# Performance work log

Measured on AMD Instinct MI355X. Metric: run time of the kernel, lower is better.

## Reference

```python
import jax, jax.numpy as jnp
import numpy as np
from jax import lax

EPOCHS = 3
N_IN, N_OUT = 20, 18
BN_EPS = 1e-5
RECT_EPS = 1e-4
TRIU = np.triu_indices(N_OUT)  # SPDVectorize upper-triangular indices


def _orth(key, n, m):
    # Stiefel init: orthonormal columns, like nn.init.orthogonal_
    q, _ = jnp.linalg.qr(jax.random.normal(key, (n, m), dtype=jnp.float32))
    return q


def setup_inputs() -> dict:
    key = jax.random.key(0)
    ks = jax.random.split(key, 8)
    bs = 2048
    f32 = jnp.float32
    return dict(
        x=jax.random.normal(ks[0], (bs, 1, 22, 438), dtype=f32),
        W1=jax.random.normal(ks[1], (22, 1, 22, 1), dtype=f32) * 0.1,
        b1=jnp.zeros((22,), f32),
        g1=jnp.ones((22,), f32), be1=jnp.zeros((22,), f32),
        W2=jax.random.normal(ks[2], (20, 22, 1, 12), dtype=f32) * 0.05,
        b2=jnp.zeros((20,), f32),
        g2=jnp.ones((20,), f32), be2=jnp.zeros((20,), f32),
        Wq=_orth(ks[3], N_IN, N_OUT),
        Wk=_orth(ks[4], N_IN, N_OUT),
        Wv=_orth(ks[5], N_IN, N_OUT),
        Wl=jax.random.normal(ks[6], (N_OUT * (N_OUT + 1) // 2 * EPOCHS, 4), dtype=f32) * 0.02,
        bl=jnp.zeros((4,), f32),
    )


def _bn(x, g, b):
    # BatchNorm2d forward in training mode (batch statistics, biased var)
    mean = x.mean(axis=(0, 2, 3), keepdims=True)
    var = ((x - mean) ** 2).mean(axis=(0, 2, 3), keepdims=True)
    return (x - mean) * lax.rsqrt(var + BN_EPS) * g[None, :, None, None] + b[None, :, None, None]


def _conv(x, w, b, pad_w):
    y = lax.conv_general_dilated(x, w, (1, 1), [(0, 0), (pad_w, pad_w)],
                                 dimension_numbers=('NCHW', 'OIHW', 'NCHW'))
    return y + b[None, :, None, None]


def _signal2spd(x):
    # x: (bs, C, L) -> trace-normalized covariance + 1e-5 * I
    L = x.shape[-1]
    xc = x - x.mean(-1, keepdims=True)
    cov = jnp.einsum('bcl,bdl->bcd', xc, xc) / (L - 1)
    cov = cov / jnp.trace(cov, axis1=-2, axis2=-1)[:, None, None]
    return cov + 1e-5 * jnp.eye(cov.shape[-1], dtype=cov.dtype)


def _patch_lens(n, epochs):
    base = n // epochs
    lens = [base] * epochs
    for i in range(n - base * epochs):
        lens[i] += 1
    return lens


def _spd_fn(t, fn):
    # SPD functional calculus via eigh (== torch.svd on SPD input)
    s, u = jnp.linalg.eigh(t)
    return jnp.einsum('...ij,...j,...kj->...ik', u, fn(s), u)


def _forward(x, W1, b1, g1, be1, W2, b2, g2, be2, Wq, Wk, Wv, Wl, bl):
    bs = x.shape[0]
    h = _bn(_conv(x, W1, b1, 0), g1, be1)          # (bs,22,1,438)
    h = _bn(_conv(h, W2, b2, 6), g2, be2)          # (bs,20,1,439)
    sig = h[:, :, 0, :]                            # squeeze -> (bs,20,439)
    covs, off = [], 0
    for L in _patch_lens(sig.shape[-1], EPOCHS):   # E2R: [147,146,146]
        covs.append(_signal2spd(sig[:, :, off:off + L]))
        off += L
    X = jnp.stack(covs, axis=1)                    # (bs,m,20,20) SPD
    # SPDTransform: W^T X W with Stiefel W (20,18)
    Q = jnp.einsum('pi,bmpq,qj->bmij', Wq, X, Wq)
    K = jnp.einsum('pi,bmpq,qj->bmij', Wk, X, Wk)
    V = jnp.einsum('pi,bmpq,qj->bmij', Wv, X, Wv)
    logQ = _spd_fn(Q, jnp.log)
    logK = _spd_fn(K, jnp.log)
    logV = _spd_fn(V, jnp.log)
    # log-Euclidean distance^2: ||log Q_j - log K_i||_F^2  (== sum of svd singvals of D D^T)
    diff = logQ[:, :, None] - logK[:, None, :]     # (bs, mq, mk, n, n)
    energy = jnp.sum(diff * diff, axis=(-2, -1))   # (bs, mq, mk)
    scores = 1.0 / (1.0 + jnp.log1p(energy))
    # torch: softmax over dim=-2 then permute(0,2,1) == softmax over K index here
    P = jax.nn.softmax(scores, axis=-1)            # (bs, mq, mk)
    mixed = jnp.einsum('bji,bipq->bjpq', P, logV)  # weighted log-Euclidean mean
    out = _spd_fn(mixed, jnp.exp)
    out = _spd_fn(out, lambda s: jnp.maximum(s, RECT_EPS))  # SPDRectified
    logO = _spd_fn(out, jnp.log)                   # SPDTangentSpace log
    vec = logO[..., TRIU[0], TRIU[1]]              # (bs, m, 171)
    return vec.reshape(bs, -1) @ Wl + bl           # (bs, 4)


def reference(x, W1, b1, g1, be1, W2, b2, g2, be2, Wq, Wk, Wv, Wl, bl):
    return _forward(x, W1, b1, g1, be1, W2, b2, g2, be2, Wq, Wk, Wv, Wl, bl)
```

## Files before the change

### kernel.cpp

```cpp
#include <hip/hip_runtime.h>
#include <math.h>

#define OFF_Y2   0
#define OFF_QKV  17981440
#define OFF_ST   (17981440 + 5971968)
#define ST_SX   0
#define ST_SXX  22
#define ST_WF   506
#define ST_BF   990
#define ST_Y2S  1012
#define ST_Y2Q  1032
#define ST_TOT  1052

#define LOGEPS -9.210340371976182f
#define NSWEEP 5
#define SHIFT  12.0f

__global__ __launch_bounds__(256) void k0_zero(float* __restrict__ st){
  for (int i = threadIdx.x; i < ST_TOT; i += 256) st[i] = 0.f;
}

__global__ __launch_bounds__(256) void k1_xstats(const float* __restrict__ x, float* __restrict__ st){
  __shared__ __align__(16) float xs[22*444];
  const float* xb = x + (size_t)blockIdx.x * (22*438);
  for (int i = threadIdx.x; i < 22*444; i += 256){
    int h = i / 444, w = i - h*444;
    xs[i] = (w < 438) ? xb[h*438 + w] : 0.f;
  }
  __syncthreads();
  for (int t = threadIdx.x; t < 275; t += 256){
    if (t < 22){
      const float4* r = (const float4*)&xs[t*444];
      float4 acc = {0.f,0.f,0.f,0.f};
      for (int w = 0; w < 111; ++w){ float4 v = r[w]; acc.x+=v.x; acc.y+=v.y; acc.z+=v.z; acc.w+=v.w; }
      atomicAdd(&st[ST_SX + t], acc.x+acc.y+acc.z+acc.w);
    } else {
      int rem = t - 22, h = 0;
      while (rem >= 22 - h){ rem -= 22 - h; ++h; }
      int h2 = h + rem;
      const float4* ra = (const float4*)&xs[h*444];
      const float4* rb = (const float4*)&xs[h2*444];
      float4 acc = {0.f,0.f,0.f,0.f};
      for (int w = 0; w < 111; ++w){
        float4 a = ra[w], b = rb[w];
        acc.x = fmaf(a.x,b.x,acc.x); acc.y = fmaf(a.y,b.y,acc.y);
        acc.z = fmaf(a.z,b.z,acc.z); acc.w = fmaf(a.w,b.w,acc.w);
      }
      atomicAdd(&st[ST_SXX + h*22 + h2], acc.x+acc.y+acc.z+acc.w);
    }
  }
}

__global__ __launch_bounds__(64) void k1b_fold(const float* __restrict__ W1, const float* __restrict__ g1,
                                               const float* __restrict__ be1, float* __restrict__ st){
  int c = threadIdx.x;
  if (c >= 22) return;
  const float invN = 1.f / (2048.f*438.f);
  float mcol[22];
  float mu0 = 0.f;
  for (int h = 0; h < 22; ++h){ mcol[h] = W1[c*22 + h]; mu0 = fmaf(mcol[h], st[ST_SX + h], mu0); }
  mu0 *= invN;
  float qf = 0.f;
  for (int h = 0; h < 22; ++h)
    for (int h2 = h; h2 < 22; ++h2){
      float w = mcol[h]*mcol[h2]*st[ST_SXX + h*22 + h2];
      qf += (h2 == h) ? w : 2.f*w;
    }
  qf *= invN;
  float var = qf - mu0*mu0;
  float a1 = g1[c] * rsqrtf(var + 1e-5f);
  for (int h = 0; h < 22; ++h) st[ST_WF + h*22 + c] = a1 * mcol[h];
  st[ST_BF + c] = be1[c] - a1 * mu0;
}

__global__ __launch_bounds__(512, 2) void k3_conv(const float* __restrict__ x, const float* __restrict__ W2,
                                                  const float* __restrict__ st, float* __restrict__ y2){
  __shared__ __align__(16) float zs[22*452 + 20];
  __shared__ __align__(16) float w2s[20*268];
  __shared__ __align__(16) float wfs[22*24];
  __shared__ float bfs[22];
  int tid = threadIdx.x;
  int n = blockIdx.x;
  for (int i = tid; i < 484; i += 512){ int h = i/22, c = i - h*22; wfs[h*24 + c] = st[ST_WF + i]; }
  for (int i = tid; i < 5280; i += 512){ int d = i/264, r = i - d*264; w2s[d*268 + r] = W2[i]; }
  if (tid < 22) bfs[tid] = st[ST_BF + tid];
  for (int i = tid; i < 22*14; i += 512){ int c = i/14, k = i - c*14; int w = (k < 6) ? k : (438 + k); zs[c*452 + w] = 0.f; }
  __syncthreads();
  if (tid < 438){
    float acc[22];
    #pragma unroll
    for (int c = 0; c < 22; ++c) acc[c] = bfs[c];
    const float* xb = x + (size_t)n*(22*438) + tid;
    #pragma unroll 1
    for (int h = 0; h < 22; ++h){
      float xv = xb[h*438];
      #pragma unroll
      for (int c = 0; c < 22; ++c) acc[c] = fmaf(wfs[h*24 + c], xv, acc[c]);
    }
    #pragma unroll
    for (int c = 0; c < 22; ++c) zs[c*452 + tid + 6] = acc[c];
  }
  __syncthreads();
  if (tid < 380){
    int chunk = tid / 20, d = tid - chunk*20;
    int w0 = chunk*24;
    float acc[24];
    #pragma unroll
    for (int jj = 0; jj < 24; ++jj) acc[jj] = 0.f;
    #pragma unroll 1
    for (int c = 0; c < 22; ++c){
      const float* zr = &zs[c*452 + w0];
      float zw[36];
      #pragma unroll
      for (int k = 0; k < 36; k += 4){ float4 v = *(const float4*)&zr[k]; zw[k]=v.x; zw[k+1]=v.y; zw[k+2]=v.z; zw[k+3]=v.w; }
      const float* wr = &w2s[d*268 + c*12];
      float wt[12];
      #pragma unroll
      for (int t = 0; t < 12; t += 4){ float4 v = *(const float4*)&wr[t]; wt[t]=v.x; wt[t+1]=v.y; wt[t+2]=v.z; wt[t+3]=v.w; }
      #pragma unroll
      for (int jj = 0; jj < 24; ++jj)
        #pragma unroll
        for (int t = 0; t < 12; ++t)
          acc[jj] = fmaf(wt[t], zw[jj+t], acc[jj]);
    }
    float* yb = y2 + (size_t)n*8780 + d*439;
    #pragma unroll
    for (int jj = 0; jj < 24; ++jj){ int w = w0 + jj; if (w < 439) yb[w] = acc[jj]; }
  }
}

__global__ __launch_bounds__(256) void k3b_y2stats(const float* __restrict__ y2, float* __restrict__ st){
  int d = blockIdx.x, chunk = blockIdx.y;
  float sum = 0.f, sq = 0.f;
  for (int n = chunk*128; n < chunk*128 + 128; ++n){
    const float* r = y2 + (size_t)n*8780 + d*439;
    for (int w = threadIdx.x; w < 439; w += 256){ float v = r[w]; sum += v; sq = fmaf(v, v, sq); }
  }
  __shared__ float red[4][2];
  for (int off = 32; off; off >>= 1){ sum += __shfl_down(sum, off); sq += __shfl_down(sq, off); }
  int wid = threadIdx.x >> 6;
  if ((threadIdx.x & 63) == 0){ red[wid][0] = sum; red[wid][1] = sq; }
  __syncthreads();
  if (threadIdx.x == 0){
    float s = 0.f, q = 0.f;
    for (int i = 0; i < 4; ++i){ s += red[i][0]; q += red[i][1]; }
    atomicAdd(&st[ST_Y2S + d], s);
    atomicAdd(&st[ST_Y2Q + d], q);
  }
}

__global__ __launch_bounds__(256) void k4_cov_qkv(const float* __restrict__ y2, const float* __restrict__ st,
    const float* __restrict__ g2, const float* __restrict__ Wq, const float* __restrict__ Wk,
    const float* __restrict__ Wv, float* __restrict__ qkv){
  __shared__ __align__(16) float ysp[3][20][148];
  __shared__ float a2s[20];
  __shared__ __align__(16) float Bt[3][18][20];
  __shared__ __align__(16) float G3[3][400];
  __shared__ __align__(16) float Tmt[3][360];
  __shared__ float musum3[3][20];
  __shared__ float rtr3[3];
  int tid = threadIdx.x, n = blockIdx.x;
  if (tid < 20){
    const float invN = 1.f/(2048.f*439.f);
    float s = st[ST_Y2S + tid]*invN;
    float q = st[ST_Y2Q + tid]*invN;
    a2s[tid] = g2[tid] * rsqrtf(q - s*s + 1e-5f);
  }
  const float* yb = y2 + (size_t)n*8780;
  for (int i = tid; i < 8780; i += 256){
    int d = i/439, w = i - d*439;
    int m = (w >= 293) ? 2 : ((w >= 147) ? 1 : 0);
    int lw = w - ((m == 2) ? 293 : ((m == 1) ? 147 : 0));
    ysp[m][d][lw] = yb[i];
  }
  if (tid < 100){
    int d = tid/5, k = tid - d*5;
    int m = (k == 0) ? 0 : ((k < 3) ? 1 : 2);
    int lw = (k == 0) ? 147 : ((k == 1 || k == 3) ? 146 : 147);
    ysp[m][d][lw] = 0.f;
  }
  __syncthreads();
  for (int i = tid; i < 1140; i += 256){
    if (i < 1080){
      int wt = i/360, r = i - wt*360; int d = r/18, jj = r - d*18;
      const float* Wm = (wt==0) ? Wq : ((wt==1) ? Wk : Wv);
      Bt[wt][jj][d] = a2s[d]*Wm[d*18 + jj];
    } else {
      int t = i - 1080; int m = t/20, d = t - m*20;
      const float4* r = (const float4*)&ysp[m][d][0];
      float4 acc = {0.f,0.f,0.f,0.f};
      #pragma unroll 1
      for (int w = 0; w < 37; ++w){ float4 v = r[w]; acc.x+=v.x; acc.y+=v.y; acc.z+=v.z; acc.w+=v.w; }
      musum3[m][d] = acc.x+acc.y+acc.z+acc.w;
    }
  }
  __syncthreads();
  for (int it = tid; it < 630; it += 256){
    int m = it/210, t = it - m*210;
    int rem = t, c = 0;
    while (rem >= 20 - c){ rem -= 20 - c; ++c; }
    int d = c + rem;
    const float4* ra = (const float4*)&ysp[m][c][0];
    const float4* rb = (const float4*)&ysp[m][d][0];
    float4 acc4 = {0.f,0.f,0.f,0.f};
    #pragma unroll 1
    for (int w = 0; w < 37; ++w){
      float4 a = ra[w], b = rb[w];
      acc4.x = fmaf(a.x,b.x,acc4.x); acc4.y = fmaf(a.y,b.y,acc4.y);
      acc4.z = fmaf(a.z,b.z,acc4.z); acc4.w = fmaf(a.w,b.w,acc4.w);
    }
    float invL = (m == 0) ? (1.f/147.f) : (1.f/146.f);
    float acc = (acc4.x+acc4.y+acc4.z+acc4.w) - musum3[m][c]*musum3[m][d]*invL;
    G3[m][c*20 + d] = acc; G3[m][d*20 + c] = acc;
  }
  __syncthreads();
  for (int wt = 0; wt < 3; ++wt){
    for (int i = tid; i < 1083; i += 256){
      if (i < 1080){
        int m = i/360, r = i - m*360; int p = r/18, jj = r - p*18;
        const float4* gr = (const float4*)&G3[m][p*20];
        const float4* br = (const float4*)&Bt[wt][jj][0];
        float4 a4 = {0.f,0.f,0.f,0.f};
        #pragma unroll
        for (int w = 0; w < 5; ++w){
          float4 a = gr[w], b = br[w];
          a4.x = fmaf(a.x,b.x,a4.x); a4.y = fmaf(a.y,b.y,a4.y);
          a4.z = fmaf(a.z,b.z,a4.z); a4.w = fmaf(a.w,b.w,a4.w);
        }
        Tmt[m][jj*20 + p] = a4.x+a4.y+a4.z+a4.w;
      } else if (wt == 0){
        int m = i - 1080;
        float tr = 0.f;
        for (int c = 0; c < 20; ++c){ float a = a2s[c]; tr = fmaf(a*a, G3[m][c*21], tr); }
        rtr3[m] = 1.f/tr;
      }
    }
    __syncthreads();
    for (int it = tid; it < 513; it += 256){
      int m = it/171, t = it - m*171;
      int rem = t, i = 0;
      while (rem >= 18 - i){ rem -= 18 - i; ++i; }
      int jj = i + rem;
      const float4* br = (const float4*)&Bt[wt][i][0];
      const float4* tr = (const float4*)&Tmt[m][jj*20];
      float4 a4 = {0.f,0.f,0.f,0.f};
      #pragma unroll
      for (int w = 0; w < 5; ++w){
        float4 a = br[w], b = tr[w];
        a4.x = fmaf(a.x,b.x,a4.x); a4.y = fmaf(a.y,b.y,a4.y);
        a4.z = fmaf(a.z,b.z,a4.z); a4.w = fmaf(a.w,b.w,a4.w);
      }
      float acc = (a4.x+a4.y+a4.z+a4.w) * rtr3[m];
      if (i == jj) acc += 1e-5f;
      float* outm = qkv + ((size_t)wt*6144 + (size_t)n*3 + m)*324;
      outm[i*18 + jj] = acc; outm[jj*18 + i] = acc;
    }
    __syncthreads();
  }
}

__global__ __launch_bounds__(256, 4) void k5_oneside(const float* __restrict__ src, float* __restrict__ dst,
    int nmat, int mode, const float* __restrict__ Wl, const float* __restrict__ bl,
    float* __restrict__ outp){
  __shared__ __align__(16) float stage[12][384];
  __shared__ __align__(16) float wls[2052];
  __shared__ float outacc[4][4];
  int tid = threadIdx.x;
  int wave = tid >> 6, lane = tid & 63;
  int g = (lane >= 54) ? 3 : (lane >= 36 ? 2 : (lane >= 18 ? 1 : 0));
  int j = lane - g*18;
  int gb = g*18;
  int slot = wave*3 + ((g < 3) ? g : 0);
  int mat = blockIdx.x*12 + wave*3 + g;
  bool act = (g < 3) && (mat < nmat);

  if (mode == 1){
    for (int i = tid; i < 2052; i += 256) wls[i] = Wl[i];
    if (tid < 16) outacc[tid >> 2][tid & 3] = 0.f;
  }

  float b[18];
  float sh = (mode == 1) ? SHIFT : 0.f;
  if (act){
    const float* s = src + (size_t)mat*324 + j*18;
    #pragma unroll
    for (int i = 0; i < 18; ++i) b[i] = s[i] + ((i == j) ? sh : 0.f);
  } else {
    #pragma unroll
    for (int i = 0; i < 18; ++i) b[i] = (i == j) ? 1.f : 0.f;
  }
  float nrm;
  { float n0 = 0.f, n1 = 0.f;
    #pragma unroll
    for (int k = 0; k < 18; k += 2){ n0 = fmaf(b[k],b[k],n0); n1 = fmaf(b[k+1],b[k+1],n1); }
    nrm = n0 + n1; }

  #pragma unroll 1
  for (int sweep = 0; sweep < NSWEEP; ++sweep){
    #pragma unroll
    for (int r = 0; r < 17; ++r){
      int xx = j - 1 - r; if (xx < 0) xx += 17;
      int v = r + 17 - xx; if (v >= 17) v -= 17;
      int m = (j == 0) ? (1 + r) : ((xx == 0) ? 0 : (1 + v));
      bool isp = (j == 0) ? true : ((xx == 0) ? false : (xx <= 8));
      int plane = (gb + m) & 63;
      float rv[18];
      #pragma unroll
      for (int k = 0; k < 18; ++k) rv[k] = __shfl(b[k], plane);
      float on = __shfl(nrm, plane);
      float g0 = 0.f, g1 = 0.f;
      #pragma unroll
      for (int k = 0; k < 18; k += 2){ g0 = fmaf(b[k], rv[k], g0); g1 = fmaf(b[k+1], rv[k+1], g1); }
      float gam = g0 + g1;
      float alpha = isp ? nrm : on;
      float beta  = isp ? on  : nrm;
      float tau = (beta - alpha) * 0.5f * __builtin_amdgcn_rcpf(gam);
      float tt = __builtin_amdgcn_rcpf(fabsf(tau) + sqrtf(fmaf(tau, tau, 1.f)));
      float t = (tau >= 0.f) ? tt : -tt;
      if (!(fabsf(gam) > 1e-36f)) t = 0.f;
      float c = __builtin_amdgcn_rsqf(fmaf(t, t, 1.f));
      float s = t*c;
      nrm = fmaf(isp ? -t : t, gam, nrm);
      float sg = isp ? -s : s;
      #pragma unroll
      for (int k = 0; k < 18; ++k) b[k] = fmaf(c, b[k], sg*rv[k]);
    }
  }
  float n0 = 0.f, n1 = 0.f;
  #pragma unroll
  for (int k = 0; k < 18; k += 2){ n0 = fmaf(b[k],b[k],n0); n1 = fmaf(b[k+1],b[k+1],n1); }
  float nf = fmaxf(n0 + n1, 1e-30f);
  float fv = (mode == 0) ? (0.5f * logf(nf)) : fmaxf(sqrtf(nf) - SHIFT, LOGEPS);
  float wv = fv * __builtin_amdgcn_rcpf(nf);
  float* sp = &stage[slot][0];
  if (act){
    #pragma unroll
    for (int k = 0; k < 18; ++k) sp[k*20 + j] = b[k];
    sp[360 + j] = wv;
  }
  __syncthreads();
  if (act){
    float wr[18];
    #pragma unroll
    for (int i = 0; i < 18; ++i) wr[i] = sp[j*20 + i] * sp[360 + i];
    float frow[18];
    #pragma unroll
    for (int i2 = 0; i2 < 18; ++i2){
      const float* br = &sp[i2*20];
      float a0 = 0.f;
      #pragma unroll
      for (int k = 0; k < 16; k += 4){
        float4 v4 = *(const float4*)&br[k];
        a0 = fmaf(wr[k],   v4.x, a0); a0 = fmaf(wr[k+1], v4.y, a0);
        a0 = fmaf(wr[k+2], v4.z, a0); a0 = fmaf(wr[k+3], v4.w, a0);
      }
      a0 = fmaf(wr[16], br[16], a0);
      a0 = fmaf(wr[17], br[17], a0);
      frow[i2] = a0;
    }
    if (mode == 0){
      float* orow = dst + (size_t)mat*324 + j*18;
      #pragma unroll
      for (int i2 = 0; i2 < 18; ++i2) orow[i2] = frow[i2];
    } else {
      int base = (g*171 + j*(37 - j)/2 - j)*4;
      float o0=0.f, o1=0.f, o2=0.f, o3=0.f;
      #pragma unroll
      for (int jj = 0; jj < 18; ++jj){
        if (jj >= j){
          const float* w4 = &wls[base + jj*4];
          o0 = fmaf(frow[jj], w4[0], o0);
          o1 = fmaf(frow[jj], w4[1], o1);
          o2 = fmaf(frow[jj], w4[2], o2);
          o3 = fmaf(frow[jj], w4[3], o3);
        }
      }
      atomicAdd(&outacc[wave][0], o0);
      atomicAdd(&outacc[wave][1], o1);
      atomicAdd(&outacc[wave][2], o2);
      atomicAdd(&outacc[wave][3], o3);
    }
  }
  if (mode == 1){
    __syncthreads();
    if (tid < 16){
      int bi = tid >> 2, o = tid & 3;
      outp[(blockIdx.x*4 + bi)*4 + o] = outacc[bi][o] + bl[o];
    }
  }
}

__global__ __launch_bounds__(128) void k6_attnmix(const float* __restrict__ logs, float* __restrict__ mixed){
  __shared__ float lq[972], lk[972], lv[972];
  __shared__ float ew[2][9];
  __shared__ float P[9];
  int b = blockIdx.x, tid = threadIdx.x;
  const float* q  = logs + (size_t)b*972;
  const float* k_ = logs + 1990656 + (size_t)b*972;
  const float* v_ = logs + 3981312 + (size_t)b*972;
  for (int i = tid; i < 972; i += 128){ lq[i] = q[i]; lk[i] = k_[i]; lv[i] = v_[i]; }
  __syncthreads();
  float e[9] = {0.f,0.f,0.f,0.f,0.f,0.f,0.f,0.f,0.f};
  for (int x = tid; x < 324; x += 128){
    float q0 = lq[x], q1 = lq[324+x], q2 = lq[648+x];
    float k0 = lk[x], k1 = lk[324+x], k2 = lk[648+x];
    float d;
    d = q0-k0; e[0] = fmaf(d,d,e[0]);
    d = q0-k1; e[1] = fmaf(d,d,e[1]);
    d = q0-k2; e[2] = fmaf(d,d,e[2]);
    d = q1-k0; e[3] = fmaf(d,d,e[3]);
    d = q1-k1; e[4] = fmaf(d,d,e[4]);
    d = q1-k2; e[5] = fmaf(d,d,e[5]);
    d = q2-k0; e[6] = fmaf(d,d,e[6]);
    d = q2-k1; e[7] = fmaf(d,d,e[7]);
    d = q2-k2; e[8] = fmaf(d,d,e[8]);
  }
  #pragma unroll
  for (int p = 0; p < 9; ++p)
    for (int off = 32; off; off >>= 1) e[p] += __shfl_down(e[p], off);
  if ((tid & 63) == 0){
    #pragma unroll
    for (int p = 0; p < 9; ++p) ew[tid >> 6][p] = e[p];
  }
  __syncthreads();
  if (tid < 3){
    float en0 = ew[0][tid*3+0] + ew[1][tid*3+0];
    float en1 = ew[0][tid*3+1] + ew[1][tid*3+1];
    float en2 = ew[0][tid*3+2] + ew[1][tid*3+2];
    float s0 = 1.f/(1.f + log1pf(en0));
    float s1 = 1.f/(1.f + log1pf(en1));
    float s2 = 1.f/(1.f + log1pf(en2));
    float mx = fmaxf(s0, fmaxf(s1, s2));
    float e0 = expf(s0-mx), e1 = expf(s1-mx), e2 = expf(s2-mx);
    float inv = 1.f/(e0+e1+e2);
    P[tid*3+0] = e0*inv; P[tid*3+1] = e1*inv; P[tid*3+2] = e2*inv;
  }
  __syncthreads();
  float p00=P[0],p01=P[1],p02=P[2],p10=P[3],p11=P[4],p12=P[5],p20=P[6],p21=P[7],p22=P[8];
  float* mb = mixed + (size_t)b*972;
  for (int x = tid; x < 324; x += 128){
    float v0 = lv[x], v1 = lv[324+x], v2 = lv[648+x];
    mb[x]     = p00*v0 + p01*v1 + p02*v2;
    mb[324+x] = p10*v0 + p11*v1 + p12*v2;
    mb[648+x] = p20*v0 + p21*v1 + p22*v2;
  }
}

extern "C" void kernel_launch(void* const* d_in, const int* in_sizes, int n_in,
                              void* d_out, int out_size, void* d_ws, size_t ws_size,
                              hipStream_t stream){
  (void)in_sizes; (void)n_in; (void)out_size; (void)ws_size;
  const float* x   = (const float*)d_in[0];
  const float* W1  = (const float*)d_in[1];
  const float* g1  = (const float*)d_in[3];
  const float* be1 = (const float*)d_in[4];
  const float* W2  = (const float*)d_in[5];
  const float* g2  = (const float*)d_in[7];
  const float* Wq  = (const float*)d_in[9];
  const float* Wk  = (const float*)d_in[10];
  const float* Wv  = (const float*)d_in[11];
  const float* Wl  = (const float*)d_in[12];
  const float* bl  = (const float*)d_in[13];
  float* ws    = (float*)d_ws;
  float* y2    = ws + OFF_Y2;
  float* qkv   = ws + OFF_QKV;
  float* logs  = ws + OFF_Y2;
  float* mixed = ws + OFF_QKV;
  float* st    = ws + OFF_ST;
  float* outp  = (float*)d_out;

  k0_zero    <<<dim3(1),      dim3(256), 0, stream>>>(st);
  k1_xstats  <<<dim3(2048),   dim3(256), 0, stream>>>(x, st);
  k1b_fold   <<<dim3(1),      dim3(64),  0, stream>>>(W1, g1, be1, st);
  k3_conv    <<<dim3(2048),   dim3(512), 0, stream>>>(x, W2, st, y2);
  k3b_y2stats<<<dim3(20,16),  dim3(256), 0, stream>>>(y2, st);
  k4_cov_qkv <<<dim3(2048),   dim3(256), 0, stream>>>(y2, st, g2, Wq, Wk, Wv, qkv);
  k5_oneside <<<dim3(1536),   dim3(256), 0, stream>>>(qkv, logs, 18432, 0, nullptr, nullptr, nullptr);
  k6_attnmix <<<dim3(2048),   dim3(128), 0, stream>>>(logs, mixed);
  k5_oneside <<<dim3(512),    dim3(256), 0, stream>>>(mixed, nullptr, 6144, 1, Wl, bl, outp);
}
```

Before: 749.4 us.

## Fuse y2 BN statistics into conv and split conv output channels across blocks

Removes the separate k3b_y2stats kernel by accumulating the per-channel sum and sum-of-squares of y2 inside the conv epilogue, first with shared-memory atomics and then with global atomics. This saves one full re-read of y2 from memory. The conv grid is also split in two along output channels (10 per block, 256 threads), and the first conv stage is vectorised with float2 loads. The cost of the split is that the first-stage 1x1 conv is recomputed in each half, and global atomic traffic rises.

```diff
diff --git a/kernel.cpp b/kernel.cpp
--- a/kernel.cpp
+++ b/kernel.cpp
@@ -73,36 +73,44 @@
   st[ST_BF + c] = be1[c] - a1 * mu0;
 }
 
-__global__ __launch_bounds__(512, 2) void k3_conv(const float* __restrict__ x, const float* __restrict__ W2,
-                                                  const float* __restrict__ st, float* __restrict__ y2){
+__global__ __launch_bounds__(256, 3) void k3_conv(const float* __restrict__ x, const float* __restrict__ W2,
+                                                  float* __restrict__ st, float* __restrict__ y2){
   __shared__ __align__(16) float zs[22*452 + 20];
-  __shared__ __align__(16) float w2s[20*268];
+  __shared__ __align__(16) float w2s[10*268];
   __shared__ __align__(16) float wfs[22*24];
   __shared__ float bfs[22];
+  __shared__ float sloc[10], qloc[10];
   int tid = threadIdx.x;
   int n = blockIdx.x;
-  for (int i = tid; i < 484; i += 512){ int h = i/22, c = i - h*22; wfs[h*24 + c] = st[ST_WF + i]; }
-  for (int i = tid; i < 5280; i += 512){ int d = i/264, r = i - d*264; w2s[d*268 + r] = W2[i]; }
+  int dbase = blockIdx.y * 10;
+  for (int i = tid; i < 484; i += 256){ int h = i/22, c = i - h*22; wfs[h*24 + c] = st[ST_WF + i]; }
+  for (int i = tid; i < 2640; i += 256){ int dl = i/264, r = i - dl*264; w2s[dl*268 + r] = W2[(dbase + dl)*264 + r]; }
   if (tid < 22) bfs[tid] = st[ST_BF + tid];
-  for (int i = tid; i < 22*14; i += 512){ int c = i/14, k = i - c*14; int w = (k < 6) ? k : (438 + k); zs[c*452 + w] = 0.f; }
-  __syncthreads();
-  if (tid < 438){
-    float acc[22];
-    #pragma unroll
-    for (int c = 0; c < 22; ++c) acc[c] = bfs[c];
-    const float* xb = x + (size_t)n*(22*438) + tid;
+  if (tid < 10){ sloc[tid] = 0.f; qloc[tid] = 0.f; }
+  for (int i = tid; i < 22*14; i += 256){ int c = i/14, k = i - c*14; int w = (k < 6) ? k : (438 + k); zs[c*452 + w] = 0.f; }
+  __syncthreads();
+  if (tid < 219){
+    float2 acc[22];
+    #pragma unroll
+    for (int c = 0; c < 22; ++c){ float b = bfs[c]; acc[c].x = b; acc[c].y = b; }
+    const float* xb = x + (size_t)n*(22*438) + 2*tid;
     #pragma unroll 1
     for (int h = 0; h < 22; ++h){
-      float xv = xb[h*438];
-      #pragma unroll
-      for (int c = 0; c < 22; ++c) acc[c] = fmaf(wfs[h*24 + c], xv, acc[c]);
-    }
-    #pragma unroll
-    for (int c = 0; c < 22; ++c) zs[c*452 + tid + 6] = acc[c];
-  }
-  __syncthreads();
-  if (tid < 380){
-    int chunk = tid / 20, d = tid - chunk*20;
+      float2 xv = *(const float2*)&xb[h*438];
+      #pragma unroll
+      for (int c = 0; c < 22; ++c){
+        float w = wfs[h*24 + c];
+        acc[c].x = fmaf(w, xv.x, acc[c].x);
+        acc[c].y = fmaf(w, xv.y, acc[c].y);
+      }
+    }
+    #pragma unroll
+    for (int c = 0; c < 22; ++c) *(float2*)&zs[c*452 + 6 + 2*tid] = acc[c];
+  }
+  __syncthreads();
+  if (tid < 190){
+    int chunk = tid / 10, dl = tid - chunk*10;
+    int d = dbase + dl;
     int w0 = chunk*24;
     float acc[24];
     #pragma unroll
@@ -113,7 +121,7 @@
       float zw[36];
       #pragma unroll
       for (int k = 0; k < 36; k += 4){ float4 v = *(const float4*)&zr[k]; zw[k]=v.x; zw[k+1]=v.y; zw[k+2]=v.z; zw[k+3]=v.w; }
-      const float* wr = &w2s[d*268 + c*12];
+      const float* wr = &w2s[dl*268 + c*12];
       float wt[12];
       #pragma unroll
       for (int t = 0; t < 12; t += 4){ float4 v = *(const float4*)&wr[t]; wt[t]=v.x; wt[t+1]=v.y; wt[t+2]=v.z; wt[t+3]=v.w; }
@@ -124,28 +132,19 @@
           acc[jj] = fmaf(wt[t], zw[jj+t], acc[jj]);
     }
     float* yb = y2 + (size_t)n*8780 + d*439;
-    #pragma unroll
-    for (int jj = 0; jj < 24; ++jj){ int w = w0 + jj; if (w < 439) yb[w] = acc[jj]; }
-  }
-}
-
-__global__ __launch_bounds__(256) void k3b_y2stats(const float* __restrict__ y2, float* __restrict__ st){
-  int d = blockIdx.x, chunk = blockIdx.y;
-  float sum = 0.f, sq = 0.f;
-  for (int n = chunk*128; n < chunk*128 + 128; ++n){
-    const float* r = y2 + (size_t)n*8780 + d*439;
-    for (int w = threadIdx.x; w < 439; w += 256){ float v = r[w]; sum += v; sq = fmaf(v, v, sq); }
-  }
-  __shared__ float red[4][2];
-  for (int off = 32; off; off >>= 1){ sum += __shfl_down(sum, off); sq += __shfl_down(sq, off); }
-  int wid = threadIdx.x >> 6;
-  if ((threadIdx.x & 63) == 0){ red[wid][0] = sum; red[wid][1] = sq; }
-  __syncthreads();
-  if (threadIdx.x == 0){
     float s = 0.f, q = 0.f;
-    for (int i = 0; i < 4; ++i){ s += red[i][0]; q += red[i][1]; }
-    atomicAdd(&st[ST_Y2S + d], s);
-    atomicAdd(&st[ST_Y2Q + d], q);
+    #pragma unroll
+    for (int jj = 0; jj < 24; ++jj){
+      int w = w0 + jj;
+      if (w < 439){ yb[w] = acc[jj]; s += acc[jj]; q = fmaf(acc[jj], acc[jj], q); }
+    }
+    atomicAdd(&sloc[dl], s);
+    atomicAdd(&qloc[dl], q);
+  }
+  __syncthreads();
+  if (tid < 10){
+    atomicAdd(&st[ST_Y2S + dbase + tid], sloc[tid]);
+    atomicAdd(&st[ST_Y2Q + dbase + tid], qloc[tid]);
   }
 }
 
@@ -469,13 +468,12 @@
   float* st    = ws + OFF_ST;
   float* outp  = (float*)d_out;
 
-  k0_zero    <<<dim3(1),      dim3(256), 0, stream>>>(st);
-  k1_xstats  <<<dim3(2048),   dim3(256), 0, stream>>>(x, st);
-  k1b_fold   <<<dim3(1),      dim3(64),  0, stream>>>(W1, g1, be1, st);
-  k3_conv    <<<dim3(2048),   dim3(512), 0, stream>>>(x, W2, st, y2);
-  k3b_y2stats<<<dim3(20,16),  dim3(256), 0, stream>>>(y2, st);
-  k4_cov_qkv <<<dim3(2048),   dim3(256), 0, stream>>>(y2, st, g2, Wq, Wk, Wv, qkv);
-  k5_oneside <<<dim3(1536),   dim3(256), 0, stream>>>(qkv, logs, 18432, 0, nullptr, nullptr, nullptr);
-  k6_attnmix <<<dim3(2048),   dim3(128), 0, stream>>>(logs, mixed);
-  k5_oneside <<<dim3(512),    dim3(256), 0, stream>>>(mixed, nullptr, 6144, 1, Wl, bl, outp);
-}
+  k0_zero    <<<dim3(1),       dim3(256), 0, stream>>>(st);
+  k1_xstats  <<<dim3(2048),    dim3(256), 0, stream>>>(x, st);
+  k1b_fold   <<<dim3(1),       dim3(64),  0, stream>>>(W1, g1, be1, st);
+  k3_conv    <<<dim3(2048,2),  dim3(256), 0, stream>>>(x, W2, st, y2);
+  k4_cov_qkv <<<dim3(2048),    dim3(256), 0, stream>>>(y2, st, g2, Wq, Wk, Wv, qkv);
+  k5_oneside <<<dim3(1536),    dim3(256), 0, stream>>>(qkv, logs, 18432, 0, nullptr, nullptr, nullptr);
+  k6_attnmix <<<dim3(2048),    dim3(128), 0, stream>>>(logs, mixed);
+  k5_oneside <<<dim3(512),     dim3(256), 0, stream>>>(mixed, nullptr, 6144, 1, Wl, bl, outp);
+}
```

After: 749.1 us. Within noise of the previous version (-0.0%).
